# Optimization experiments

Hardware: AMD Instinct MI355X
Metric: run time of the kernel (lower is better)

The kernel has to match this reference:

```python
import jax, jax.numpy as jnp
import numpy as np

EPS = 0.01
EXPD_WEIGHT = 1.0
COMP_WEIGHT = 1.0
NUM_CLASSES = 32
M, D = 262144, 128


def setup_inputs() -> dict:
    key = jax.random.key(0)
    k1, k2 = jax.random.split(key)
    cls_score = jax.random.normal(k1, (M, D), dtype=jnp.float32)
    label = jax.random.randint(k2, (M,), 0, NUM_CLASSES)
    return {"cls_score": cls_score, "label": label}


def _logdet(X):
    sgn, ld = jnp.linalg.slogdet(X)
    return sgn * ld


def reference(cls_score, label):
    m, d = cls_score.shape
    m_f = jnp.asarray(m, cls_score.dtype)
    # expansion term: logdet(c * Z^T Z) / 2, c = d / (m * eps)
    c = d / (m_f * EPS)
    cov = cls_score.T @ cls_score  # [d, d]
    loss_expd = _logdet(c * cov) / 2.0

    # compression term: sum_j m_j/(2m) * logdet(c_j * Z_j^T Z_j)
    def per_class(j):
        mask = (label == j).astype(cls_score.dtype)  # [m]
        m_j = mask.sum()
        safe_mj = jnp.maximum(m_j, 1.0)
        c_j = d / (safe_mj * EPS)
        # Z_j^T Z_j == (mask * Z)^T Z, honoring the boolean subset without gather
        cov_j = (cls_score * mask[:, None]).T @ cls_score  # [d, d]
        ld_j = _logdet(c_j * cov_j)
        return jnp.where(m_j > 0, ld_j * m_j / (2.0 * m_f), 0.0)

    comps = jax.lax.map(per_class, jnp.arange(NUM_CLASSES))  # [J]
    loss_comp = comps.sum()

    # MCR2Loss.forward with return_all=False
    return loss_comp * COMP_WEIGHT - loss_expd * EXPD_WEIGHT
```

## Files before the change

kernel.cpp:

```cpp
#include <hip/hip_runtime.h>
#include <math.h>

#define D 128
#define NCLS 32
#define TSLOT 16
#define CHUNK 256

typedef float f32x16 __attribute__((ext_vector_type(16)));
typedef short bf16x8 __attribute__((ext_vector_type(8)));

__global__ void zero_k(int* hist) {
  int t = threadIdx.x;
  if (t < NCLS) hist[t] = 0;
}

__global__ __launch_bounds__(64) void hist_blk_k(const int* __restrict__ label, int M,
                                                 int NB, int* __restrict__ blkhist_t,
                                                 int* __restrict__ hist) {
  __shared__ int h[NCLS];
  const int lane = threadIdx.x;
  const int b = blockIdx.x;
  if (lane < NCLS) h[lane] = 0;
  __syncthreads();
  const int s0 = b * CHUNK;
#pragma unroll
  for (int it = 0; it < CHUNK / 64; ++it) {
    int i = s0 + it * 64 + lane;
    if (i < M) atomicAdd(&h[label[i]], 1);
  }
  __syncthreads();
  if (lane < NCLS) {
    blkhist_t[lane * NB + b] = h[lane];
    atomicAdd(&hist[lane], h[lane]);
  }
}

__global__ void prefix_k(const int* __restrict__ hist, int* __restrict__ cstart) {
  if (threadIdx.x == 0) {
    int run = 0;
    for (int j = 0; j < NCLS; ++j) { cstart[j] = run; run += hist[j]; }
    cstart[NCLS] = run;
  }
}

__global__ __launch_bounds__(64) void base_k(const int* __restrict__ blkhist_t,
                                             const int* __restrict__ cstart, int NB,
                                             int* __restrict__ base_t) {
  const int j = blockIdx.x;
  const int lane = threadIdx.x;
  const int K = (NB + 63) / 64;
  int vals[32];
  int run = 0;
  for (int k = 0; k < K; ++k) {
    int b = lane * K + k;
    int v = (b < NB) ? blkhist_t[j * NB + b] : 0;
    vals[k] = v;
    run += v;
  }
  int incl = run;
  for (int off = 1; off < 64; off <<= 1) {
    int o = __shfl_up(incl, off);
    if (lane >= off) incl += o;
  }
  int pos = cstart[j] + (incl - run);
  for (int k = 0; k < K; ++k) {
    int b = lane * K + k;
    if (b < NB) base_t[j * NB + b] = pos;
    pos += vals[k];
  }
}

__global__ __launch_bounds__(64) void scatter2_k(const int* __restrict__ label, int M,
                                                 int NB, const int* __restrict__ base_t,
                                                 int* __restrict__ idxbuf) {
  __shared__ int cur[NCLS];
  const int b = blockIdx.x;
  const int lane = threadIdx.x;
  if (lane < NCLS) cur[lane] = base_t[lane * NB + b];
  __syncthreads();
  const int s0 = b * CHUNK;
#pragma unroll
  for (int it = 0; it < CHUNK / 64; ++it) {
    int i = s0 + it * 64 + lane;
    int j = (i < M) ? label[i] : -1;
    unsigned long long mask = 0;
#pragma unroll
    for (int q = 0; q < NCLS; ++q) {
      unsigned long long mm = __ballot(j == q);
      if (j == q) mask = mm;
    }
    if (j >= 0) {
      int myoff = __popcll(mask & ((1ull << lane) - 1ull));
      int basec = cur[j];
      idxbuf[basec + myoff] = i;
      if (myoff == 0) cur[j] = basec + __popcll(mask);
    }
    __syncthreads();
  }
}

__device__ inline void bsplit(float x, short& hi, short& lo) {
  unsigned u = __float_as_uint(x);
  unsigned rh = u + 0x7fffu + ((u >> 16) & 1u);
  unsigned short h = (unsigned short)(rh >> 16);
  float hf = __uint_as_float((unsigned)h << 16);
  float l = x - hf;
  unsigned ul = __float_as_uint(l);
  unsigned rl = ul + 0x7fffu + ((ul >> 16) & 1u);
  hi = (short)h;
  lo = (short)(rl >> 16);
}

__global__ __launch_bounds__(512, 4) void cov_k(const float* __restrict__ Z,
                                                const int* __restrict__ idxbuf,
                                                const int* __restrict__ hist,
                                                const int* __restrict__ cstart,
                                                float* __restrict__ partials) {
  __shared__ __attribute__((aligned(16))) char arena[66048];

  const int b = blockIdx.x;
  const int cls = b / TSLOT, slot = b % TSLOT;
  const int t = threadIdx.x;
  const int lane = t & 63;
  const int w = t >> 6;
  const int r = w & 3;
  const int pass = w >> 2;
  const int col4 = t & 31;
  const int rg = t >> 5;

  const int mj = hist[cls];
  const int seg0 = cstart[cls];
  const int segend = seg0 + mj;
  const int nch = (mj + 63) / 64;

  f32x16 acc[4];
#pragma unroll
  for (int c = 0; c < 4; ++c)
#pragma unroll
    for (int i = 0; i < 16; ++i) acc[c][i] = 0.f;

  const int pcol = r * 32 + (lane & 31);
  const int h = lane >> 5;
  const int aswz = (pcol & 7) << 4;
  char* const bbase = arena + (pass ? 16384 : 0);

  float4 pv[4];
  {
    const int ch = slot;
    const int r0 = seg0 + ch * 64;
#pragma unroll
    for (int i = 0; i < 4; ++i) {
      int gr = r0 + rg * 4 + i;
      if (ch < nch && gr < segend) {
        int ridx = idxbuf[gr];
        pv[i] = *(const float4*)(Z + (size_t)ridx * D + col4 * 4);
      } else {
        pv[i] = make_float4(0.f, 0.f, 0.f, 0.f);
      }
    }
  }

  for (int ch = slot; ch < nch; ch += TSLOT) {
    __syncthreads();
    {
      float xs[4][4];
      xs[0][0] = pv[0].x; xs[0][1] = pv[0].y; xs[0][2] = pv[0].z; xs[0][3] = pv[0].w;
      xs[1][0] = pv[1].x; xs[1][1] = pv[1].y; xs[1][2] = pv[1].z; xs[1][3] = pv[1].w;
      xs[2][0] = pv[2].x; xs[2][1] = pv[2].y; xs[2][2] = pv[2].z; xs[2][3] = pv[2].w;
      xs[3][0] = pv[3].x; xs[3][1] = pv[3].y; xs[3][2] = pv[3].z; xs[3][3] = pv[3].w;
#pragma unroll
      for (int j = 0; j < 4; ++j) {
        short h0, h1, h2, h3, l0, l1, l2, l3;
        bsplit(xs[0][j], h0, l0);
        bsplit(xs[1][j], h1, l1);
        bsplit(xs[2][j], h2, l2);
        bsplit(xs[3][j], h3, l3);
        const int cc = col4 * 4 + j;
        const int off = cc * 128 + ((rg * 8) ^ ((cc & 7) << 4));
        *(short4*)(arena + off) = make_short4(h0, h1, h2, h3);
        *(short4*)(arena + 16384 + off) = make_short4(l0, l1, l2, l3);
      }
    }
    __syncthreads();
    {
      const int chn = ch + TSLOT;
      const int r0 = seg0 + chn * 64;
#pragma unroll
      for (int i = 0; i < 4; ++i) {
        int gr = r0 + rg * 4 + i;
        if (chn < nch && gr < segend) {
          int ridx = idxbuf[gr];
          pv[i] = *(const float4*)(Z + (size_t)ridx * D + col4 * 4);
        } else {
          pv[i] = make_float4(0.f, 0.f, 0.f, 0.f);
        }
      }
    }
#pragma unroll
    for (int kk = 0; kk < 4; ++kk) {
      const int koff = kk * 32 + h * 16;
      bf16x8 a = *(const bf16x8*)(arena + pcol * 128 + (koff ^ aswz));
#pragma unroll
      for (int c = 0; c < 4; ++c) {
        const int qcol = c * 32 + (lane & 31);
        bf16x8 bb = *(const bf16x8*)(bbase + qcol * 128 + (koff ^ ((qcol & 7) << 4)));
        acc[c] = __builtin_amdgcn_mfma_f32_32x32x16_bf16(a, bb, acc[c], 0, 0, 0);
      }
    }
  }

  __syncthreads();
  float* g2 = (float*)arena;
  if (pass == 1) {
#pragma unroll
    for (int c = 0; c < 4; ++c)
#pragma unroll
      for (int i = 0; i < 16; ++i) {
        int prow = r * 32 + (i & 3) + 8 * (i >> 2) + 4 * h;
        int qcol = c * 32 + (lane & 31);
        g2[prow * 129 + qcol] = acc[c][i];
      }
  }
  __syncthreads();
  if (pass == 0) {
    size_t base = (size_t)b * (D * D);
#pragma unroll
    for (int c = 0; c < 4; ++c)
#pragma unroll
      for (int i = 0; i < 16; ++i) {
        int prow = r * 32 + (i & 3) + 8 * (i >> 2) + 4 * h;
        int qcol = c * 32 + (lane & 31);
        float v = acc[c][i] + g2[prow * 129 + qcol] + g2[qcol * 129 + prow];
        partials[base + (size_t)prow * D + qcol] = v;
      }
  }
}

__global__ void reduce_k(const float* __restrict__ partials, float* __restrict__ covs) {
  int e = blockIdx.x * blockDim.x + threadIdx.x;
  double tot = 0.0;
  for (int j = 0; j < NCLS; ++j) {
    double s = 0.0;
    for (int t = 0; t < TSLOT; ++t)
      s += (double)partials[(size_t)(j * TSLOT + t) * (D * D) + e];
    covs[(size_t)j * (D * D) + e] = (float)s;
    tot += s;
  }
  covs[(size_t)NCLS * (D * D) + e] = (float)tot;
}

__global__ __launch_bounds__(256, 1) void chol_k(const float* __restrict__ covs,
                                                 const int* __restrict__ hist,
                                                 int Mtot, double* __restrict__ results) {
  __shared__ float As[128][132];
  __shared__ float PlT[32][36];
  __shared__ float invd[32];
  __shared__ float colbuf[32];
  __shared__ double red[64];
  __shared__ __attribute__((aligned(16))) short Thi[96 * 40];
  __shared__ __attribute__((aligned(16))) short Tlo[96 * 40];
  const int j = blockIdx.x;
  const float* A = covs + (size_t)j * (D * D);
  const int tid = threadIdx.x;
  const int lane = tid & 63;
  const int wv = tid >> 6;

#pragma unroll
  for (int it = 0; it < 16; ++it) {
    int e = it * 1024 + tid * 4;
    int r = e >> 7, c = e & 127;
    *(float4*)&As[r][c] = *(const float4*)&A[e];
  }
  __syncthreads();

  double lda = 0.0;
#pragma unroll 1
  for (int p = 0; p < 4; ++p) {
    const int pbase = p * 32;
    const int N2 = 96 - pbase;
    if (wv == 0) {
      const int l = lane & 31;
      float row[32];
#pragma unroll
      for (int c4 = 0; c4 < 8; ++c4) {
        float4 v = *(const float4*)&As[pbase + l][pbase + c4 * 4];
        row[c4 * 4 + 0] = v.x; row[c4 * 4 + 1] = v.y;
        row[c4 * 4 + 2] = v.z; row[c4 * 4 + 3] = v.w;
      }
      float mypiv = 1.f, myinv = 0.f;
#pragma unroll
      for (int k = 0; k < 32; ++k) {
        colbuf[l] = row[k];
        float cb[32];
#pragma unroll
        for (int q = 0; q < 8; ++q) {
          float4 v = *(const float4*)&colbuf[q * 4];
          cb[q * 4 + 0] = v.x; cb[q * 4 + 1] = v.y;
          cb[q * 4 + 2] = v.z; cb[q * 4 + 3] = v.w;
        }
        float piv = cb[k];
        float inv = rsqrtf(piv);
        inv = inv * (1.5f - 0.5f * piv * inv * inv);
        if (lane == k) { mypiv = piv; myinv = inv; }
        float tmul = row[k] * (inv * inv);
#pragma unroll
        for (int c = k + 1; c < 32; ++c)
          row[c] = fmaf(-tmul, cb[c], row[c]);
        row[k] *= inv;
      }
      if (lane < 32) {
#pragma unroll
        for (int c = 0; c < 32; ++c) PlT[c][lane] = row[c];
        invd[lane] = myinv;
      }
      lda += log((double)mypiv);
    }
    __syncthreads();
    if (tid < N2) {
      const int R = pbase + 32 + tid;
      float s[32];
#pragma unroll
      for (int c4 = 0; c4 < 8; ++c4) {
        float4 v = *(const float4*)&As[R][pbase + c4 * 4];
        s[c4 * 4 + 0] = v.x; s[c4 * 4 + 1] = v.y;
        s[c4 * 4 + 2] = v.z; s[c4 * 4 + 3] = v.w;
      }
#pragma unroll
      for (int i = 0; i < 32; ++i) {
        float xi = s[i] * invd[i];
        s[i] = xi;
#pragma unroll
        for (int jj = i + 1; jj < 32; ++jj)
          s[jj] = fmaf(-xi, PlT[i][jj], s[jj]);
      }
      unsigned hp[16], lp[16];
#pragma unroll
      for (int q = 0; q < 16; ++q) {
        short ha, la, hb, lb;
        bsplit(s[2 * q], ha, la);
        bsplit(s[2 * q + 1], hb, lb);
        hp[q] = (unsigned)(unsigned short)ha | ((unsigned)(unsigned short)hb << 16);
        lp[q] = (unsigned)(unsigned short)la | ((unsigned)(unsigned short)lb << 16);
      }
#pragma unroll
      for (int q = 0; q < 4; ++q) {
        *(int4*)&Thi[tid * 40 + q * 8] =
            make_int4(hp[4 * q], hp[4 * q + 1], hp[4 * q + 2], hp[4 * q + 3]);
        *(int4*)&Tlo[tid * 40 + q * 8] =
            make_int4(lp[4 * q], lp[4 * q + 1], lp[4 * q + 2], lp[4 * q + 3]);
      }
    }
    __syncthreads();
    const int nstr = N2 >> 5;
    if (wv < nstr) {
      const int l31 = lane & 31;
      const int h = lane >> 5;
      const int arow = wv * 32 + l31;
#pragma unroll 1
      for (int ct = 0; ct < nstr; ++ct) {
        const int brow = ct * 32 + l31;
        f32x16 acc;
#pragma unroll
        for (int i = 0; i < 16; ++i) acc[i] = 0.f;
#pragma unroll
        for (int ks = 0; ks < 2; ++ks) {
          const int off = ks * 16 + h * 8;
          bf16x8 ahi = *(const bf16x8*)&Thi[arow * 40 + off];
          bf16x8 alo = *(const bf16x8*)&Tlo[arow * 40 + off];
          bf16x8 bhi = *(const bf16x8*)&Thi[brow * 40 + off];
          bf16x8 blo = *(const bf16x8*)&Tlo[brow * 40 + off];
          acc = __builtin_amdgcn_mfma_f32_32x32x16_bf16(ahi, bhi, acc, 0, 0, 0);
          acc = __builtin_amdgcn_mfma_f32_32x32x16_bf16(ahi, blo, acc, 0, 0, 0);
          acc = __builtin_amdgcn_mfma_f32_32x32x16_bf16(alo, bhi, acc, 0, 0, 0);
        }
#pragma unroll
        for (int i = 0; i < 16; ++i) {
          int rr = pbase + 32 + wv * 32 + (i & 3) + 8 * (i >> 2) + 4 * h;
          int cc = pbase + 32 + ct * 32 + l31;
          As[rr][cc] -= acc[i];
        }
      }
    }
    __syncthreads();
  }

  if (wv == 0) red[lane] = lda;
  __syncthreads();
  if (tid == 0) {
    double lsum = 0.0;
    for (int i = 0; i < 64; ++i) lsum += red[i];
    if (j < NCLS) {
      int mj = hist[j];
      double res = 0.0;
      if (mj > 0) {
        double cj = (double)D / ((double)mj * 0.01);
        res = ((double)D * log(cj) + lsum) * (double)mj / (2.0 * (double)Mtot);
      }
      results[j] = res;
    } else {
      double c = (double)D / ((double)Mtot * 0.01);
      results[NCLS] = ((double)D * log(c) + lsum) * 0.5;
    }
  }
}

__global__ void final_k(const double* __restrict__ results, float* __restrict__ out) {
  if (threadIdx.x == 0 && blockIdx.x == 0) {
    double s = 0.0;
    for (int j = 0; j < NCLS; ++j) s += results[j];
    out[0] = (float)(s - results[NCLS]);
  }
}

extern "C" void kernel_launch(void* const* d_in, const int* in_sizes, int n_in,
                              void* d_out, int out_size, void* d_ws, size_t ws_size,
                              hipStream_t stream) {
  const float* Z = (const float*)d_in[0];
  const int* label = (const int*)d_in[1];
  const int Mtot = in_sizes[1];
  float* out = (float*)d_out;
  const int NB = (Mtot + CHUNK - 1) / CHUNK;

  char* ws = (char*)d_ws;
  int* hist = (int*)(ws + 0);
  int* cstart = (int*)(ws + 256);
  double* results = (double*)(ws + 512);
  int* idxbuf = (int*)(ws + 1024);
  float* partials = (float*)(ws + 1024 + (size_t)Mtot * sizeof(int));
  float* covs = partials + (size_t)NCLS * TSLOT * D * D;
  int* blkhist_t = (int*)partials;
  int* base_t = blkhist_t + (size_t)NCLS * NB;

  zero_k<<<1, 64, 0, stream>>>(hist);
  hist_blk_k<<<NB, 64, 0, stream>>>(label, Mtot, NB, blkhist_t, hist);
  prefix_k<<<1, 64, 0, stream>>>(hist, cstart);
  base_k<<<NCLS, 64, 0, stream>>>(blkhist_t, cstart, NB, base_t);
  scatter2_k<<<NB, 64, 0, stream>>>(label, Mtot, NB, base_t, idxbuf);
  cov_k<<<NCLS * TSLOT, 512, 0, stream>>>(Z, idxbuf, hist, cstart, partials);
  reduce_k<<<(D * D) / 256, 256, 0, stream>>>(partials, covs);
  chol_k<<<NCLS + 1, 256, 0, stream>>>(covs, hist, Mtot, results);
  final_k<<<1, 64, 0, stream>>>(results, out);
}
```

Before: 126.3 us.

## Retile covariance MFMA work per wave and drop LDS cross-pass reduction

New measurement: 125.1 us. No clear change (-1.0%).

```diff
diff --git a/kernel.cpp b/kernel.cpp
--- a/kernel.cpp
+++ b/kernel.cpp
@@ -116,33 +116,36 @@
                                                 const int* __restrict__ hist,
                                                 const int* __restrict__ cstart,
                                                 float* __restrict__ partials) {
-  __shared__ __attribute__((aligned(16))) char arena[66048];
+  __shared__ __attribute__((aligned(16))) char arena[2 * 16896];
+  char* const ThiB = arena;
+  char* const TloB = arena + 16896;
 
   const int b = blockIdx.x;
   const int cls = b / TSLOT, slot = b % TSLOT;
   const int t = threadIdx.x;
   const int lane = t & 63;
   const int w = t >> 6;
-  const int r = w & 3;
-  const int pass = w >> 2;
+  const int r = w >> 1;
+  const int cp = (w & 1) * 2;
+
   const int col4 = t & 31;
   const int rg = t >> 5;
+  const int wbase0 = (((rg >> 2) * 4 + (col4 >> 3)) * 2 + ((rg >> 1) & 1)) * 528 +
+                     (col4 & 7) * 16 + (rg & 1) * 8;
 
   const int mj = hist[cls];
   const int seg0 = cstart[cls];
   const int segend = seg0 + mj;
   const int nch = (mj + 63) / 64;
 
-  f32x16 acc[4];
-#pragma unroll
-  for (int c = 0; c < 4; ++c)
-#pragma unroll
-    for (int i = 0; i < 16; ++i) acc[c][i] = 0.f;
-
-  const int pcol = r * 32 + (lane & 31);
-  const int h = lane >> 5;
-  const int aswz = (pcol & 7) << 4;
-  char* const bbase = arena + (pass ? 16384 : 0);
+  f32x16 acc[2];
+#pragma unroll
+  for (int u = 0; u < 2; ++u)
+#pragma unroll
+    for (int i = 0; i < 16; ++i) acc[u][i] = 0.f;
+
+  const int n = lane & 31;
+  const int poff = ((n >> 2) + 8 * (n & 3)) * 16 + (lane >> 5) * 528;
 
   float4 pv[4];
   {
@@ -175,10 +178,8 @@
         bsplit(xs[1][j], h1, l1);
         bsplit(xs[2][j], h2, l2);
         bsplit(xs[3][j], h3, l3);
-        const int cc = col4 * 4 + j;
-        const int off = cc * 128 + ((rg * 8) ^ ((cc & 7) << 4));
-        *(short4*)(arena + off) = make_short4(h0, h1, h2, h3);
-        *(short4*)(arena + 16384 + off) = make_short4(l0, l1, l2, l3);
+        *(short4*)(ThiB + wbase0 + j * 128) = make_short4(h0, h1, h2, h3);
+        *(short4*)(TloB + wbase0 + j * 128) = make_short4(l0, l1, l2, l3);
       }
     }
     __syncthreads();
@@ -198,42 +199,30 @@
     }
 #pragma unroll
     for (int kk = 0; kk < 4; ++kk) {
-      const int koff = kk * 32 + h * 16;
-      bf16x8 a = *(const bf16x8*)(arena + pcol * 128 + (koff ^ aswz));
-#pragma unroll
-      for (int c = 0; c < 4; ++c) {
-        const int qcol = c * 32 + (lane & 31);
-        bf16x8 bb = *(const bf16x8*)(bbase + qcol * 128 + (koff ^ ((qcol & 7) << 4)));
-        acc[c] = __builtin_amdgcn_mfma_f32_32x32x16_bf16(a, bb, acc[c], 0, 0, 0);
-      }
-    }
-  }
-
-  __syncthreads();
-  float* g2 = (float*)arena;
-  if (pass == 1) {
-#pragma unroll
-    for (int c = 0; c < 4; ++c)
-#pragma unroll
-      for (int i = 0; i < 16; ++i) {
-        int prow = r * 32 + (i & 3) + 8 * (i >> 2) + 4 * h;
-        int qcol = c * 32 + (lane & 31);
-        g2[prow * 129 + qcol] = acc[c][i];
-      }
-  }
-  __syncthreads();
-  if (pass == 0) {
-    size_t base = (size_t)b * (D * D);
-#pragma unroll
-    for (int c = 0; c < 4; ++c)
-#pragma unroll
-      for (int i = 0; i < 16; ++i) {
-        int prow = r * 32 + (i & 3) + 8 * (i >> 2) + 4 * h;
-        int qcol = c * 32 + (lane & 31);
-        float v = acc[c][i] + g2[prow * 129 + qcol] + g2[qcol * 129 + prow];
-        partials[base + (size_t)prow * D + qcol] = v;
-      }
-  }
+      const int ab = (kk * 4 + r) * 1056 + poff;
+      bf16x8 ahi = *(const bf16x8*)(ThiB + ab);
+      bf16x8 alo = *(const bf16x8*)(TloB + ab);
+#pragma unroll
+      for (int u = 0; u < 2; ++u) {
+        const int bb = (kk * 4 + cp + u) * 1056 + poff;
+        bf16x8 bhi = *(const bf16x8*)(ThiB + bb);
+        bf16x8 blo = *(const bf16x8*)(TloB + bb);
+        acc[u] = __builtin_amdgcn_mfma_f32_32x32x16_bf16(ahi, bhi, acc[u], 0, 0, 0);
+        acc[u] = __builtin_amdgcn_mfma_f32_32x32x16_bf16(ahi, blo, acc[u], 0, 0, 0);
+        acc[u] = __builtin_amdgcn_mfma_f32_32x32x16_bf16(alo, bhi, acc[u], 0, 0, 0);
+      }
+    }
+  }
+
+  size_t base = (size_t)b * (D * D);
+#pragma unroll
+  for (int u = 0; u < 2; ++u)
+#pragma unroll
+    for (int i = 0; i < 16; ++i) {
+      int prow = r * 32 + (i & 3) + 8 * (i >> 2) + 4 * (lane >> 5);
+      int qcol = (cp + u) * 32 + (lane & 31);
+      partials[base + (size_t)prow * D + qcol] = acc[u][i];
+    }
 }
 
 __global__ void reduce_k(const float* __restrict__ partials, float* __restrict__ covs) {
```
